# Optimization experiments

Measured on AMD Instinct MI355X. Metric: run time of the kernel, lower is better.

The kernel has to match this reference:

```python
import jax, jax.numpy as jnp
import numpy as np

SIZE_U = 1000
SIZE_V = 1000
D = 128          # input_dim
NW = 2           # num_weights
NC = 2           # num_classes
M_EXTRA = 16     # extra rows beyond size_u+size_v (the 'M' slice)


def setup_inputs() -> dict:
    key = jax.random.key(0)
    k1, k2, k3 = jax.random.split(key, 3)
    feature = jax.random.normal(k1, (SIZE_U + SIZE_V + M_EXTRA, D), dtype=jnp.float32)
    # kaiming-uniform-like scale for the bilinear weights and classifier
    weight = jax.random.uniform(k2, (NW, D, D), dtype=jnp.float32,
                                minval=-1.0, maxval=1.0) * float(np.sqrt(6.0 / D))
    weight_classifier = jax.random.uniform(k3, (NW, NC), dtype=jnp.float32,
                                           minval=-1.0, maxval=1.0) * float(np.sqrt(6.0 / NW))
    return {"feature": feature, "weight": weight, "weight_classifier": weight_classifier}


def reference(feature, weight, weight_classifier):
    # dropout treated as identity (inference mode)
    lnc = feature[:SIZE_U]                       # [U, D]
    dis = feature[SIZE_U:SIZE_U + SIZE_V]        # [V, D]
    M = feature[SIZE_U + SIZE_V:]                # [M_EXTRA, D]

    # Per-weight bilinear score: scores[u,v,k] = lnc[u] @ W_k @ dis[v]
    # Reordered (project-then-score) to avoid the O(U*V*D^2) naive expansion,
    # but math is identical to the original pairwise loop.
    proj = jnp.einsum('kde,ud->kue', weight, lnc)          # [NW, U, D]
    scores = jnp.einsum('kue,ve->uvk', proj, dis)          # [U, V, NW]
    scores = scores.reshape(SIZE_U * SIZE_V, NW)           # matches meshgrid('ij') flatten order

    outputs = jax.nn.relu(scores @ weight_classifier)      # [U*V, NC]

    # Replicated pair features, as returned by the original module
    lnc_rep = jnp.repeat(lnc, SIZE_V, axis=0)              # [U*V, D] (row_idx varies slowest)
    dis_rep = jnp.tile(dis, (SIZE_U, 1))                   # [U*V, D]
    return (outputs, lnc_rep, dis_rep, M)
```

## Files before the change

kernel.cpp:

```cpp
#include <hip/hip_runtime.h>

#define SIZE_U 1000
#define SIZE_V 1000
#define DIM    128
#define M_EXTRA 16

typedef float f32x4 __attribute__((ext_vector_type(4)));

#define OUT_LNC_OFF 2000000L
#define OUT_DIS_OFF 130000000L
#define OUT_M_OFF   258000000L

__global__ __launch_bounds__(256) void bilinear_v8_kernel(
    const float* __restrict__ feature,
    const float* __restrict__ weight,
    const float* __restrict__ wc,
    float* __restrict__ out)
{
    const int b = blockIdx.x;
    const int t = threadIdx.x;

    if (b == 4000) {
        const f32x4* src = (const f32x4*)(feature + (size_t)(SIZE_U + SIZE_V) * DIM);
        f32x4* dst = (f32x4*)(out + OUT_M_OFF);
        for (int i = t; i < (M_EXTRA * DIM) / 4; i += 256) dst[i] = src[i];
        return;
    }

    const int g    = b >> 3;
    const int role = g & 1;
    const int j    = (g >> 1) * 8 + (b & 7);
    const int u    = j >> 1;
    const int r0   = (j & 1) * 500;
    const int r1   = r0 + 500;

    const int c  = t & 31;
    const int rg = t >> 5;
    const f32x4* dis4 = (const f32x4*)(feature + (size_t)SIZE_U * DIM);
    const size_t rowbase = (size_t)u * SIZE_V;

    if (role == 0) {
        const f32x4 lnc4 = ((const f32x4*)(feature + (size_t)u * DIM))[c];
        f32x4* lr = (f32x4*)(out + OUT_LNC_OFF) + rowbase * (DIM / 4);
        #pragma unroll 8
        for (int r = r0 + rg; r < r1; r += 8)
            lr[r * 32 + c] = lnc4;

        f32x4* dr = (f32x4*)(out + OUT_DIS_OFF) + rowbase * (DIM / 4);
        #pragma unroll 8
        for (int r = r0 + rg; r < r1; r += 8) {
            const int idx = r * 32 + c;
            dr[idx] = dis4[idx];
        }
    } else {
        __shared__ float lnc_s[DIM];
        __shared__ float proj_s[2][DIM];
        __shared__ float q_s[2][DIM];

        if (t < DIM) lnc_s[t] = feature[(size_t)u * DIM + t];
        __syncthreads();

        {
            const int k = t >> 7, e = t & 127;
            const float* wk = weight + (size_t)k * DIM * DIM + e;
            float acc = 0.f;
            #pragma unroll 8
            for (int d = 0; d < DIM; ++d)
                acc = fmaf(wk[(size_t)d * DIM], lnc_s[d], acc);
            proj_s[k][e] = acc;
        }
        __syncthreads();

        {
            const int cc = t >> 7, e = t & 127;
            q_s[cc][e] = wc[cc] * proj_s[0][e] + wc[2 + cc] * proj_s[1][e];
        }
        __syncthreads();

        const f32x4 q0 = ((const f32x4*)q_s[0])[c];
        const f32x4 q1 = ((const f32x4*)q_s[1])[c];
        float2* outp = (float2*)out;

        #pragma unroll 4
        for (int r = r0 + rg; r < r1; r += 8) {
            const f32x4 dv = dis4[r * 32 + c];
            float t0 = dv.x * q0.x + dv.y * q0.y + dv.z * q0.z + dv.w * q0.w;
            float t1 = dv.x * q1.x + dv.y * q1.y + dv.z * q1.z + dv.w * q1.w;
            #pragma unroll
            for (int off = 16; off; off >>= 1) {
                t0 += __shfl_xor(t0, off);
                t1 += __shfl_xor(t1, off);
            }
            if (c == 0)
                outp[rowbase + r] = make_float2(t0 > 0.f ? t0 : 0.f,
                                                t1 > 0.f ? t1 : 0.f);
        }
    }
}

extern "C" void kernel_launch(void* const* d_in, const int* in_sizes, int n_in,
                              void* d_out, int out_size, void* d_ws, size_t ws_size,
                              hipStream_t stream) {
    const float* feature = (const float*)d_in[0];
    const float* weight  = (const float*)d_in[1];
    const float* wc      = (const float*)d_in[2];
    float* out = (float*)d_out;

    bilinear_v8_kernel<<<4001, 256, 0, stream>>>(feature, weight, wc, out);
}
```

Baseline: 193.9 us.

## Use persistent blocks with atomic work-stealing over finer-grained copy and score tasks

Replaces the fixed 4001-block grid with 2048 persistent blocks that grab task ids from a global atomic counter, which is reset by a memset before each launch. The copy work is split into finer tasks: each 125-row chunk copies either the lnc or the dis stream. Compute tasks are interleaved one in every nine ids. The aim is better load balance and steadier write bandwidth for the huge replicated output. In exchange it adds an atomic, extra block barriers per task, and a memset launch.

After: 269.4 us. 1.39x slower.

```diff
diff --git a/kernel.cpp b/kernel.cpp
--- a/kernel.cpp
+++ b/kernel.cpp
@@ -11,90 +11,106 @@
 #define OUT_DIS_OFF 130000000L
 #define OUT_M_OFF   258000000L
 
-__global__ __launch_bounds__(256) void bilinear_v8_kernel(
+#define N_TOTAL 18001
+
+__global__ __launch_bounds__(256) void bilinear_v9_kernel(
     const float* __restrict__ feature,
     const float* __restrict__ weight,
     const float* __restrict__ wc,
-    float* __restrict__ out)
+    float* __restrict__ out,
+    int* __restrict__ counter)
 {
-    const int b = blockIdx.x;
-    const int t = threadIdx.x;
-
-    if (b == 4000) {
-        const f32x4* src = (const f32x4*)(feature + (size_t)(SIZE_U + SIZE_V) * DIM);
-        f32x4* dst = (f32x4*)(out + OUT_M_OFF);
-        for (int i = t; i < (M_EXTRA * DIM) / 4; i += 256) dst[i] = src[i];
-        return;
-    }
-
-    const int g    = b >> 3;
-    const int role = g & 1;
-    const int j    = (g >> 1) * 8 + (b & 7);
-    const int u    = j >> 1;
-    const int r0   = (j & 1) * 500;
-    const int r1   = r0 + 500;
-
+    const int t  = threadIdx.x;
     const int c  = t & 31;
     const int rg = t >> 5;
     const f32x4* dis4 = (const f32x4*)(feature + (size_t)SIZE_U * DIM);
-    const size_t rowbase = (size_t)u * SIZE_V;
 
-    if (role == 0) {
-        const f32x4 lnc4 = ((const f32x4*)(feature + (size_t)u * DIM))[c];
-        f32x4* lr = (f32x4*)(out + OUT_LNC_OFF) + rowbase * (DIM / 4);
-        #pragma unroll 8
-        for (int r = r0 + rg; r < r1; r += 8)
-            lr[r * 32 + c] = lnc4;
+    __shared__ int   s_id;
+    __shared__ float lnc_s[DIM];
+    __shared__ float proj_s[2][DIM];
+    __shared__ float q_s[2][DIM];
 
-        f32x4* dr = (f32x4*)(out + OUT_DIS_OFF) + rowbase * (DIM / 4);
-        #pragma unroll 8
-        for (int r = r0 + rg; r < r1; r += 8) {
-            const int idx = r * 32 + c;
-            dr[idx] = dis4[idx];
-        }
-    } else {
-        __shared__ float lnc_s[DIM];
-        __shared__ float proj_s[2][DIM];
-        __shared__ float q_s[2][DIM];
+    while (true) {
+        if (t == 0) s_id = atomicAdd(counter, 1);
+        __syncthreads();
+        const int id = s_id;
+        if (id >= N_TOTAL) break;
 
-        if (t < DIM) lnc_s[t] = feature[(size_t)u * DIM + t];
-        __syncthreads();
+        if (id == N_TOTAL - 1) {
+            const f32x4* src = (const f32x4*)(feature + (size_t)(SIZE_U + SIZE_V) * DIM);
+            f32x4* dst = (f32x4*)(out + OUT_M_OFF);
+            for (int i = t; i < (M_EXTRA * DIM) / 4; i += 256) dst[i] = src[i];
+        } else if (id % 9 == 8) {
+            const int sid = id / 9;
+            const int u   = sid >> 1;
+            const int r0  = (sid & 1) * 500;
+            const int r1  = r0 + 500;
+            const size_t rowbase = (size_t)u * SIZE_V;
 
-        {
-            const int k = t >> 7, e = t & 127;
-            const float* wk = weight + (size_t)k * DIM * DIM + e;
-            float acc = 0.f;
-            #pragma unroll 8
-            for (int d = 0; d < DIM; ++d)
-                acc = fmaf(wk[(size_t)d * DIM], lnc_s[d], acc);
-            proj_s[k][e] = acc;
+            if (t < DIM) lnc_s[t] = feature[(size_t)u * DIM + t];
+            __syncthreads();
+
+            {
+                const int k = t >> 7, e = t & 127;
+                const float* wk = weight + (size_t)k * DIM * DIM + e;
+                float acc = 0.f;
+                #pragma unroll 8
+                for (int d = 0; d < DIM; ++d)
+                    acc = fmaf(wk[(size_t)d * DIM], lnc_s[d], acc);
+                proj_s[k][e] = acc;
+            }
+            __syncthreads();
+
+            {
+                const int cc = t >> 7, e = t & 127;
+                q_s[cc][e] = wc[cc] * proj_s[0][e] + wc[2 + cc] * proj_s[1][e];
+            }
+            __syncthreads();
+
+            const f32x4 q0 = ((const f32x4*)q_s[0])[c];
+            const f32x4 q1 = ((const f32x4*)q_s[1])[c];
+            float2* outp = (float2*)out;
+
+            #pragma unroll 4
+            for (int r = r0 + rg; r < r1; r += 8) {
+                const f32x4 dv = dis4[r * 32 + c];
+                float t0 = dv.x * q0.x + dv.y * q0.y + dv.z * q0.z + dv.w * q0.w;
+                float t1 = dv.x * q1.x + dv.y * q1.y + dv.z * q1.z + dv.w * q1.w;
+                #pragma unroll
+                for (int off = 16; off; off >>= 1) {
+                    t0 += __shfl_xor(t0, off);
+                    t1 += __shfl_xor(t1, off);
+                }
+                if (c == 0)
+                    outp[rowbase + r] = make_float2(t0 > 0.f ? t0 : 0.f,
+                                                    t1 > 0.f ? t1 : 0.f);
+            }
+        } else {
+            const int cid  = (id / 9) * 8 + (id % 9);
+            const int u    = cid >> 4;
+            const int rem  = cid & 15;
+            const int strm = rem >> 3;
+            const int q    = rem & 7;
+            const int r0   = q * 125;
+            const int r1   = r0 + 125;
+            const size_t rowbase = (size_t)u * SIZE_V;
+
+            if (strm == 0) {
+                const f32x4 lnc4 = ((const f32x4*)(feature + (size_t)u * DIM))[c];
+                f32x4* lr = (f32x4*)(out + OUT_LNC_OFF) + rowbase * (DIM / 4);
+                #pragma unroll 4
+                for (int r = r0 + rg; r < r1; r += 8)
+                    lr[r * 32 + c] = lnc4;
+            } else {
+                f32x4* dr = (f32x4*)(out + OUT_DIS_OFF) + rowbase * (DIM / 4);
+                #pragma unroll 4
+                for (int r = r0 + rg; r < r1; r += 8) {
+                    const int idx = r * 32 + c;
+                    dr[idx] = dis4[idx];
+                }
+            }
         }
         __syncthreads();
-
-        {
-            const int cc = t >> 7, e = t & 127;
-            q_s[cc][e] = wc[cc] * proj_s[0][e] + wc[2 + cc] * proj_s[1][e];
-        }
-        __syncthreads();
-
-        const f32x4 q0 = ((const f32x4*)q_s[0])[c];
-        const f32x4 q1 = ((const f32x4*)q_s[1])[c];
-        float2* outp = (float2*)out;
-
-        #pragma unroll 4
-        for (int r = r0 + rg; r < r1; r += 8) {
-            const f32x4 dv = dis4[r * 32 + c];
-            float t0 = dv.x * q0.x + dv.y * q0.y + dv.z * q0.z + dv.w * q0.w;
-            float t1 = dv.x * q1.x + dv.y * q1.y + dv.z * q1.z + dv.w * q1.w;
-            #pragma unroll
-            for (int off = 16; off; off >>= 1) {
-                t0 += __shfl_xor(t0, off);
-                t1 += __shfl_xor(t1, off);
-            }
-            if (c == 0)
-                outp[rowbase + r] = make_float2(t0 > 0.f ? t0 : 0.f,
-                                                t1 > 0.f ? t1 : 0.f);
-        }
     }
 }
 
@@ -105,6 +121,8 @@
     const float* weight  = (const float*)d_in[1];
     const float* wc      = (const float*)d_in[2];
     float* out = (float*)d_out;
+    int* counter = (int*)d_ws;
 
-    bilinear_v8_kernel<<<4001, 256, 0, stream>>>(feature, weight, wc, out);
+    hipMemsetAsync(counter, 0, sizeof(int), stream);
+    bilinear_v9_kernel<<<2048, 256, 0, stream>>>(feature, weight, wc, out, counter);
 }
```

## Split replication and scoring into separate interleaved block roles with dis reuse

Applied to the files above, without the earlier changes.

Reassigns blocks into three interleaved roles: lnc replication in quarter-row chunks, dis replication where each block loads a 4KB slice of dis once and writes it to 50 destination rows, and the bilinear score computation. This removes repeated reads of dis from global/L2 for every output row and balances the work per block across the now larger grid. The store-bound replication dominates, so any gain depends on how much read traffic and block imbalance limited the previous version.

After: 231.3 us. 1.19x slower.

```diff
diff --git a/kernel.cpp b/kernel.cpp
--- a/kernel.cpp
+++ b/kernel.cpp
@@ -11,7 +11,7 @@
 #define OUT_DIS_OFF 130000000L
 #define OUT_M_OFF   258000000L
 
-__global__ __launch_bounds__(256) void bilinear_v8_kernel(
+__global__ __launch_bounds__(256) void bilinear_v10_kernel(
     const float* __restrict__ feature,
     const float* __restrict__ weight,
     const float* __restrict__ wc,
@@ -20,81 +20,91 @@
     const int b = blockIdx.x;
     const int t = threadIdx.x;
 
-    if (b == 4000) {
+    if (b == 8500) {
         const f32x4* src = (const f32x4*)(feature + (size_t)(SIZE_U + SIZE_V) * DIM);
         f32x4* dst = (f32x4*)(out + OUT_M_OFF);
         for (int i = t; i < (M_EXTRA * DIM) / 4; i += 256) dst[i] = src[i];
         return;
     }
 
-    const int g    = b >> 3;
-    const int role = g & 1;
-    const int j    = (g >> 1) * 8 + (b & 7);
-    const int u    = j >> 1;
-    const int r0   = (j & 1) * 500;
-    const int r1   = r0 + 500;
-
+    const int g = b / 17;
+    const int k = b % 17;
     const int c  = t & 31;
     const int rg = t >> 5;
     const f32x4* dis4 = (const f32x4*)(feature + (size_t)SIZE_U * DIM);
+
+    if (k < 8) {
+        const int id = g * 8 + k;
+        const int u  = id >> 2;
+        const int r0 = (id & 3) * 250;
+        const f32x4 lnc4 = ((const f32x4*)(feature + (size_t)u * DIM))[c];
+        f32x4* lr = (f32x4*)(out + OUT_LNC_OFF) + (size_t)u * SIZE_V * (DIM / 4);
+        #pragma unroll 8
+        for (int r = r0 + rg; r < r0 + 250; r += 8)
+            lr[r * 32 + c] = lnc4;
+        return;
+    }
+
+    if (k < 13) {
+        const int id = g * 5 + (k - 8);
+        const int rb = id / 20;
+        const int u0 = (id % 20) * 50;
+        const f32x4 dv = dis4[rb * 256 + t];
+        f32x4* db = (f32x4*)(out + OUT_DIS_OFF);
+        const size_t base = (size_t)rb * 256 + t;
+        #pragma unroll 5
+        for (int u = u0; u < u0 + 50; ++u)
+            db[(size_t)u * (SIZE_V * DIM / 4) + base] = dv;
+        return;
+    }
+
+    const int id = g * 4 + (k - 13);
+    const int u  = id >> 1;
+    const int r0 = (id & 1) * 500;
+    const int r1 = r0 + 500;
     const size_t rowbase = (size_t)u * SIZE_V;
 
-    if (role == 0) {
-        const f32x4 lnc4 = ((const f32x4*)(feature + (size_t)u * DIM))[c];
-        f32x4* lr = (f32x4*)(out + OUT_LNC_OFF) + rowbase * (DIM / 4);
+    __shared__ float lnc_s[DIM];
+    __shared__ float proj_s[2][DIM];
+    __shared__ float q_s[2][DIM];
+
+    if (t < DIM) lnc_s[t] = feature[(size_t)u * DIM + t];
+    __syncthreads();
+
+    {
+        const int kk = t >> 7, e = t & 127;
+        const float* wk = weight + (size_t)kk * DIM * DIM + e;
+        float acc = 0.f;
         #pragma unroll 8
-        for (int r = r0 + rg; r < r1; r += 8)
-            lr[r * 32 + c] = lnc4;
+        for (int d = 0; d < DIM; ++d)
+            acc = fmaf(wk[(size_t)d * DIM], lnc_s[d], acc);
+        proj_s[kk][e] = acc;
+    }
+    __syncthreads();
 
-        f32x4* dr = (f32x4*)(out + OUT_DIS_OFF) + rowbase * (DIM / 4);
-        #pragma unroll 8
-        for (int r = r0 + rg; r < r1; r += 8) {
-            const int idx = r * 32 + c;
-            dr[idx] = dis4[idx];
+    {
+        const int cc = t >> 7, e = t & 127;
+        q_s[cc][e] = wc[cc] * proj_s[0][e] + wc[2 + cc] * proj_s[1][e];
+    }
+    __syncthreads();
+
+    const f32x4 q0 = ((const f32x4*)q_s[0])[c];
+    const f32x4 q1 = ((const f32x4*)q_s[1])[c];
+    float2* outp = (float2*)out;
+
+    #pragma unroll 4
+    for (int r = r0 + rg; r < r1; r += 8) {
+        const f32x4 dv = dis4[r * 32 + c];
+        float t0 = dv.x * q0.x + dv.y * q0.y + dv.z * q0.z + dv.w * q0.w;
+        float t1 = dv.x * q1.x + dv.y * q1.y + dv.z * q1.z + dv.w * q1.w;
+        #pragma unroll
+        for (int off = 16; off; off >>= 1) {
+            t0 += __shfl_xor(t0, off);
+            t1 += __shfl_xor(t1, off);
         }
-    } else {
-        __shared__ float lnc_s[DIM];
-        __shared__ float proj_s[2][DIM];
-        __shared__ float q_s[2][DIM];
-
-        if (t < DIM) lnc_s[t] = feature[(size_t)u * DIM + t];
-        __syncthreads();
-
-        {
-            const int k = t >> 7, e = t & 127;
-            const float* wk = weight + (size_t)k * DIM * DIM + e;
-            float acc = 0.f;
-            #pragma unroll 8
-            for (int d = 0; d < DIM; ++d)
-                acc = fmaf(wk[(size_t)d * DIM], lnc_s[d], acc);
-            proj_s[k][e] = acc;
-        }
-        __syncthreads();
-
-        {
-            const int cc = t >> 7, e = t & 127;
-            q_s[cc][e] = wc[cc] * proj_s[0][e] + wc[2 + cc] * proj_s[1][e];
-        }
-        __syncthreads();
-
-        const f32x4 q0 = ((const f32x4*)q_s[0])[c];
-        const f32x4 q1 = ((const f32x4*)q_s[1])[c];
-        float2* outp = (float2*)out;
-
-        #pragma unroll 4
-        for (int r = r0 + rg; r < r1; r += 8) {
-            const f32x4 dv = dis4[r * 32 + c];
-            float t0 = dv.x * q0.x + dv.y * q0.y + dv.z * q0.z + dv.w * q0.w;
-            float t1 = dv.x * q1.x + dv.y * q1.y + dv.z * q1.z + dv.w * q1.w;
-            #pragma unroll
-            for (int off = 16; off; off >>= 1) {
-                t0 += __shfl_xor(t0, off);
-                t1 += __shfl_xor(t1, off);
-            }
-            if (c == 0)
-                outp[rowbase + r] = make_float2(t0 > 0.f ? t0 : 0.f,
-                                                t1 > 0.f ? t1 : 0.f);
-        }
+        if (c == 0)
+            outp[rowbase + r] = make_float2(t0 > 0.f ? t0 : 0.f,
+                                            t1 > 0.f ? t1 : 0.f);
     }
 }
 
@@ -106,5 +116,5 @@
     const float* wc      = (const float*)d_in[2];
     float* out = (float*)d_out;
 
-    bilinear_v8_kernel<<<4001, 256, 0, stream>>>(feature, weight, wc, out);
+    bilinear_v10_kernel<<<8501, 256, 0, stream>>>(feature, weight, wc, out);
 }
```
